# Optimization experiments

Measured on AMD Instinct MI355X. Metric: run time of the kernel, lower is better.

Reference implementation:

```python
import jax, jax.numpy as jnp
import numpy as np

WIN = 9
PAD = WIN // 2    # floor(9/2) = 4
WIN_SIZE = WIN * WIN
EPS = 1e-05


def _box_sum(x):
    # 9x9 ones-kernel conv, stride 1, pad 4 (SAME size), NCHW with C=1
    filt = jnp.ones((1, 1, WIN, WIN), dtype=x.dtype)
    return jax.lax.conv_general_dilated(
        x, filt, window_strides=(1, 1),
        padding=[(PAD, PAD), (PAD, PAD)],
        dimension_numbers=('NCHW', 'OIHW', 'NCHW'))


def setup_inputs() -> dict:
    key = jax.random.key(0)
    k1, k2 = jax.random.split(key)
    I = jax.random.normal(k1, (8, 1, 1024, 1024), dtype=jnp.float32)
    J = jax.random.normal(k2, (8, 1, 1024, 1024), dtype=jnp.float32)
    return {"I": I, "J": J}


def reference(I, J):
    I_sum = _box_sum(I)
    J_sum = _box_sum(J)
    I2_sum = _box_sum(I * I)
    J2_sum = _box_sum(J * J)
    IJ_sum = _box_sum(I * J)

    u_I = I_sum / WIN_SIZE
    u_J = J_sum / WIN_SIZE

    cross = IJ_sum - u_J * I_sum - u_I * J_sum + u_I * u_J * WIN_SIZE
    I_var = I2_sum - 2 * u_I * I_sum + u_I * u_I * WIN_SIZE
    J_var = J2_sum - 2 * u_J * J_sum + u_J * u_J * WIN_SIZE

    cc = cross * cross / (I_var * J_var + EPS)
    return jnp.mean(cc)
```

## Files before the change

kernel.cpp:

```cpp
#include <hip/hip_runtime.h>

#define H 1024
#define W 1024
#define NIMG 8
#define TX 64
#define CY 8
#define RS_ROWS (CY + 8)
#define NBX (W / TX)
#define NBY (H / CY)
#define NBLOCKS (NBX * NBY * NIMG)
#define EPS 1e-5f

__global__ __launch_bounds__(128, 4)
void ncc_main(const float* __restrict__ I, const float* __restrict__ J,
              float* __restrict__ partial) {
  __shared__ float4 rs4[RS_ROWS][TX];
  __shared__ float  rs1[RS_ROWS][TX];

  const int tid = threadIdx.x;
  const int gx = blockIdx.x, gy = blockIdx.y, n = blockIdx.z;
  const size_t img_off = (size_t)n * H * W;

  {
    const int r  = tid >> 3;
    const int xg = tid & 7;
    const int y  = gy * CY + r - 4;
    float a[16], b[16];
    if (y >= 0 && y < H) {
      const int xbase = gx * TX + xg * 8 - 4;
      const float* Ip = I + img_off + (size_t)y * W;
      const float* Jp = J + img_off + (size_t)y * W;
      if (xbase >= 0 && xbase + 16 <= W) {
        const float4* pa = reinterpret_cast<const float4*>(Ip + xbase);
        const float4* pb = reinterpret_cast<const float4*>(Jp + xbase);
        #pragma unroll
        for (int q = 0; q < 4; ++q) {
          float4 va = pa[q], vb = pb[q];
          a[4*q+0] = va.x; a[4*q+1] = va.y; a[4*q+2] = va.z; a[4*q+3] = va.w;
          b[4*q+0] = vb.x; b[4*q+1] = vb.y; b[4*q+2] = vb.z; b[4*q+3] = vb.w;
        }
      } else {
        #pragma unroll
        for (int k = 0; k < 16; ++k) {
          int xx = xbase + k;
          bool in = (xx >= 0) && (xx < W);
          a[k] = in ? Ip[xx] : 0.0f;
          b[k] = in ? Jp[xx] : 0.0f;
        }
      }
    } else {
      #pragma unroll
      for (int k = 0; k < 16; ++k) { a[k] = 0.0f; b[k] = 0.0f; }
    }
    float sI = 0.f, sJ = 0.f, sII = 0.f, sJJ = 0.f, sIJ = 0.f;
    #pragma unroll
    for (int k = 0; k < 9; ++k) {
      sI  += a[k];        sJ  += b[k];
      sII += a[k] * a[k]; sJJ += b[k] * b[k];
      sIJ += a[k] * b[k];
    }
    const int xg8 = xg * 8;
    #pragma unroll
    for (int i = 0; i < 8; ++i) {
      if (i > 0) {
        float an = a[i+8], al = a[i-1], bn = b[i+8], bl = b[i-1];
        sI  += an - al;           sJ  += bn - bl;
        sII += an*an - al*al;     sJJ += bn*bn - bl*bl;
        sIJ += an*bn - al*bl;
      }
      const int px = xg8 + (i ^ xg);
      rs4[r][px] = make_float4(sI, sJ, sII, sJJ);
      rs1[r][px] = sIJ;
    }
  }
  __syncthreads();

  const int x  = tid & 63;
  const int h  = tid >> 6;
  const int xs = (x & ~7) | ((x ^ (x >> 3)) & 7);
  const int base = h * 4;
  float4 rows4[9]; float rows1[9];
  float wI = 0.f, wJ = 0.f, wII = 0.f, wJJ = 0.f, wIJ = 0.f;
  #pragma unroll
  for (int k = 0; k < 9; ++k) {
    rows4[k] = rs4[base + k][xs];
    rows1[k] = rs1[base + k][xs];
    wI += rows4[k].x; wJ += rows4[k].y; wII += rows4[k].z; wJJ += rows4[k].w;
    wIJ += rows1[k];
  }
  const float inv81 = 1.0f / 81.0f;
  float acc = 0.f;
  #pragma unroll
  for (int i = 0; i < 4; ++i) {
    if (i > 0) {
      float4 e4 = rs4[base + 8 + i][xs];
      float  e1 = rs1[base + 8 + i][xs];
      wI  += e4.x - rows4[i-1].x;  wJ  += e4.y - rows4[i-1].y;
      wII += e4.z - rows4[i-1].z;  wJJ += e4.w - rows4[i-1].w;
      wIJ += e1   - rows1[i-1];
    }
    float cross = fmaf(-(wI * wJ), inv81, wIJ);
    float Iv    = fmaf(-(wI * wI), inv81, wII);
    float Jv    = fmaf(-(wJ * wJ), inv81, wJJ);
    acc = fmaf(cross * cross,
               __builtin_amdgcn_rcpf(fmaf(Iv, Jv, EPS)), acc);
  }

  #pragma unroll
  for (int off = 32; off > 0; off >>= 1)
    acc += __shfl_down(acc, off, 64);
  __syncthreads();
  if ((tid & 63) == 0) rs1[0][tid >> 6] = acc;
  __syncthreads();
  if (tid == 0) {
    const int blin = blockIdx.x + NBX * (blockIdx.y + NBY * (int)blockIdx.z);
    partial[blin] = rs1[0][0] + rs1[0][1];
  }
}

__global__ __launch_bounds__(256)
void ncc_reduce(const float* __restrict__ partial, float* __restrict__ out) {
  __shared__ float red[4];
  const int tid = threadIdx.x;
  float s = 0.f;
  #pragma unroll 8
  for (int i = tid; i < NBLOCKS; i += 256) s += partial[i];
  #pragma unroll
  for (int off = 32; off > 0; off >>= 1)
    s += __shfl_down(s, off, 64);
  if ((tid & 63) == 0) red[tid >> 6] = s;
  __syncthreads();
  if (tid == 0)
    out[0] = (red[0] + red[1] + red[2] + red[3]) *
             (1.0f / (float)((size_t)NIMG * H * W));
}

extern "C" void kernel_launch(void* const* d_in, const int* in_sizes, int n_in,
                              void* d_out, int out_size, void* d_ws, size_t ws_size,
                              hipStream_t stream) {
  const float* I = (const float*)d_in[0];
  const float* J = (const float*)d_in[1];
  float* out     = (float*)d_out;
  float* partial = (float*)d_ws;

  dim3 grid(NBX, NBY, NIMG);
  hipLaunchKernelGGL(ncc_main, grid, dim3(128), 0, stream, I, J, partial);
  hipLaunchKernelGGL(ncc_reduce, dim3(1), dim3(256), 0, stream, partial, out);
}
```

Measured before the change: 112.6 us.

## Process eight row tiles per block with register double-buffered global loads

Each block now loops over eight consecutive 8-row tiles instead of handling one, which cuts the grid by eight. The global loads for the next tile are issued into a second register buffer before the current tile's horizontal and vertical sums run, so memory latency overlaps compute. The 16-row halo is still re-read for every tile, so halo traffic does not shrink. The change adds a second barrier per tile and doubles the load registers, which may reduce occupancy, and the smaller grid may leave some CUs less busy.

Result: slower. 132.1 us (+17.3%).

```diff
diff --git a/kernel.cpp b/kernel.cpp
--- a/kernel.cpp
+++ b/kernel.cpp
@@ -5,111 +5,137 @@
 #define NIMG 8
 #define TX 64
 #define CY 8
-#define RS_ROWS (CY + 8)
+#define TPB 8
 #define NBX (W / TX)
-#define NBY (H / CY)
+#define NBY (H / (CY * TPB))
 #define NBLOCKS (NBX * NBY * NIMG)
 #define EPS 1e-5f
+
+__device__ __forceinline__ void load16(const float* __restrict__ Ip,
+                                       const float* __restrict__ Jp,
+                                       int y, int xbase, bool xfast,
+                                       float* __restrict__ a,
+                                       float* __restrict__ b) {
+  if (y >= 0 && y < H) {
+    const float* Irow = Ip + (size_t)y * W;
+    const float* Jrow = Jp + (size_t)y * W;
+    if (xfast) {
+      const float4* pa = reinterpret_cast<const float4*>(Irow + xbase);
+      const float4* pb = reinterpret_cast<const float4*>(Jrow + xbase);
+      #pragma unroll
+      for (int q = 0; q < 4; ++q) {
+        float4 va = pa[q], vb = pb[q];
+        a[4*q+0]=va.x; a[4*q+1]=va.y; a[4*q+2]=va.z; a[4*q+3]=va.w;
+        b[4*q+0]=vb.x; b[4*q+1]=vb.y; b[4*q+2]=vb.z; b[4*q+3]=vb.w;
+      }
+    } else {
+      #pragma unroll
+      for (int k = 0; k < 16; ++k) {
+        int xx = xbase + k;
+        bool in = (xx >= 0) && (xx < W);
+        a[k] = in ? Irow[xx] : 0.0f;
+        b[k] = in ? Jrow[xx] : 0.0f;
+      }
+    }
+  } else {
+    #pragma unroll
+    for (int k = 0; k < 16; ++k) { a[k] = 0.0f; b[k] = 0.0f; }
+  }
+}
 
 __global__ __launch_bounds__(128, 4)
 void ncc_main(const float* __restrict__ I, const float* __restrict__ J,
               float* __restrict__ partial) {
-  __shared__ float4 rs4[RS_ROWS][TX];
-  __shared__ float  rs1[RS_ROWS][TX];
+  __shared__ float4 rs4[16][TX];
+  __shared__ float  rs1[16][TX];
 
   const int tid = threadIdx.x;
   const int gx = blockIdx.x, gy = blockIdx.y, n = blockIdx.z;
   const size_t img_off = (size_t)n * H * W;
+  const float* Ip = I + img_off;
+  const float* Jp = J + img_off;
 
-  {
-    const int r  = tid >> 3;
-    const int xg = tid & 7;
-    const int y  = gy * CY + r - 4;
-    float a[16], b[16];
-    if (y >= 0 && y < H) {
-      const int xbase = gx * TX + xg * 8 - 4;
-      const float* Ip = I + img_off + (size_t)y * W;
-      const float* Jp = J + img_off + (size_t)y * W;
-      if (xbase >= 0 && xbase + 16 <= W) {
-        const float4* pa = reinterpret_cast<const float4*>(Ip + xbase);
-        const float4* pb = reinterpret_cast<const float4*>(Jp + xbase);
-        #pragma unroll
-        for (int q = 0; q < 4; ++q) {
-          float4 va = pa[q], vb = pb[q];
-          a[4*q+0] = va.x; a[4*q+1] = va.y; a[4*q+2] = va.z; a[4*q+3] = va.w;
-          b[4*q+0] = vb.x; b[4*q+1] = vb.y; b[4*q+2] = vb.z; b[4*q+3] = vb.w;
-        }
-      } else {
-        #pragma unroll
-        for (int k = 0; k < 16; ++k) {
-          int xx = xbase + k;
-          bool in = (xx >= 0) && (xx < W);
-          a[k] = in ? Ip[xx] : 0.0f;
-          b[k] = in ? Jp[xx] : 0.0f;
-        }
-      }
-    } else {
-      #pragma unroll
-      for (int k = 0; k < 16; ++k) { a[k] = 0.0f; b[k] = 0.0f; }
-    }
-    float sI = 0.f, sJ = 0.f, sII = 0.f, sJJ = 0.f, sIJ = 0.f;
-    #pragma unroll
-    for (int k = 0; k < 9; ++k) {
-      sI  += a[k];        sJ  += b[k];
-      sII += a[k] * a[k]; sJJ += b[k] * b[k];
-      sIJ += a[k] * b[k];
-    }
-    const int xg8 = xg * 8;
-    #pragma unroll
-    for (int i = 0; i < 8; ++i) {
-      if (i > 0) {
-        float an = a[i+8], al = a[i-1], bn = b[i+8], bl = b[i-1];
-        sI  += an - al;           sJ  += bn - bl;
-        sII += an*an - al*al;     sJJ += bn*bn - bl*bl;
-        sIJ += an*bn - al*bl;
-      }
-      const int px = xg8 + (i ^ xg);
-      rs4[r][px] = make_float4(sI, sJ, sII, sJJ);
-      rs1[r][px] = sIJ;
-    }
-  }
-  __syncthreads();
+  const int r  = tid >> 3;
+  const int xg = tid & 7;
+  const int xg8 = xg * 8;
+  const int xbase = gx * TX + xg8 - 4;
+  const bool xfast = (xbase >= 0) && (xbase + 16 <= W);
+  const int x  = tid & 63;
+  const int hh = tid >> 6;
+  const int xs = (x & ~7) | ((x ^ (x >> 3)) & 7);
+  const int pbase = hh * 4;
 
-  const int x  = tid & 63;
-  const int h  = tid >> 6;
-  const int xs = (x & ~7) | ((x ^ (x >> 3)) & 7);
-  const int base = h * 4;
-  float4 rows4[9]; float rows1[9];
-  float wI = 0.f, wJ = 0.f, wII = 0.f, wJJ = 0.f, wIJ = 0.f;
-  #pragma unroll
-  for (int k = 0; k < 9; ++k) {
-    rows4[k] = rs4[base + k][xs];
-    rows1[k] = rs1[base + k][xs];
-    wI += rows4[k].x; wJ += rows4[k].y; wII += rows4[k].z; wJJ += rows4[k].w;
-    wIJ += rows1[k];
-  }
+  const int y0 = gy * (CY * TPB);
+  float abuf[2][16], bbuf[2][16];
+  load16(Ip, Jp, y0 + r - 4, xbase, xfast, abuf[0], bbuf[0]);
+
   const float inv81 = 1.0f / 81.0f;
   float acc = 0.f;
+
   #pragma unroll
-  for (int i = 0; i < 4; ++i) {
-    if (i > 0) {
-      float4 e4 = rs4[base + 8 + i][xs];
-      float  e1 = rs1[base + 8 + i][xs];
-      wI  += e4.x - rows4[i-1].x;  wJ  += e4.y - rows4[i-1].y;
-      wII += e4.z - rows4[i-1].z;  wJJ += e4.w - rows4[i-1].w;
-      wIJ += e1   - rows1[i-1];
+  for (int t = 0; t < TPB; ++t) {
+    const int cb = t & 1, nb = cb ^ 1;
+    if (t < TPB - 1)
+      load16(Ip, Jp, y0 + (t+1)*CY + r - 4, xbase, xfast, abuf[nb], bbuf[nb]);
+
+    {
+      const float* a = abuf[cb];
+      const float* b = bbuf[cb];
+      float sI=0.f, sJ=0.f, sII=0.f, sJJ=0.f, sIJ=0.f;
+      #pragma unroll
+      for (int k = 0; k < 9; ++k) {
+        sI  += a[k];        sJ  += b[k];
+        sII += a[k]*a[k];   sJJ += b[k]*b[k];
+        sIJ += a[k]*b[k];
+      }
+      #pragma unroll
+      for (int i = 0; i < 8; ++i) {
+        if (i > 0) {
+          float an=a[i+8], al=a[i-1], bn=b[i+8], bl=b[i-1];
+          sI  += an - al;         sJ  += bn - bl;
+          sII += an*an - al*al;   sJJ += bn*bn - bl*bl;
+          sIJ += an*bn - al*bl;
+        }
+        const int px = xg8 + (i ^ xg);
+        rs4[r][px] = make_float4(sI, sJ, sII, sJJ);
+        rs1[r][px] = sIJ;
+      }
     }
-    float cross = fmaf(-(wI * wJ), inv81, wIJ);
-    float Iv    = fmaf(-(wI * wI), inv81, wII);
-    float Jv    = fmaf(-(wJ * wJ), inv81, wJJ);
-    acc = fmaf(cross * cross,
-               __builtin_amdgcn_rcpf(fmaf(Iv, Jv, EPS)), acc);
+    __syncthreads();
+
+    {
+      float4 rows4[9]; float rows1[9];
+      float wI=0.f, wJ=0.f, wII=0.f, wJJ=0.f, wIJ=0.f;
+      #pragma unroll
+      for (int k = 0; k < 9; ++k) {
+        rows4[k] = rs4[pbase + k][xs];
+        rows1[k] = rs1[pbase + k][xs];
+        wI += rows4[k].x; wJ += rows4[k].y;
+        wII += rows4[k].z; wJJ += rows4[k].w;
+        wIJ += rows1[k];
+      }
+      #pragma unroll
+      for (int i = 0; i < 4; ++i) {
+        if (i > 0) {
+          float4 e4 = rs4[pbase + 8 + i][xs];
+          float  e1 = rs1[pbase + 8 + i][xs];
+          wI  += e4.x - rows4[i-1].x;  wJ  += e4.y - rows4[i-1].y;
+          wII += e4.z - rows4[i-1].z;  wJJ += e4.w - rows4[i-1].w;
+          wIJ += e1   - rows1[i-1];
+        }
+        float cross = fmaf(-(wI * wJ), inv81, wIJ);
+        float Iv    = fmaf(-(wI * wI), inv81, wII);
+        float Jv    = fmaf(-(wJ * wJ), inv81, wJJ);
+        acc = fmaf(cross * cross,
+                   __builtin_amdgcn_rcpf(fmaf(Iv, Jv, EPS)), acc);
+      }
+    }
+    __syncthreads();
   }
 
   #pragma unroll
   for (int off = 32; off > 0; off >>= 1)
     acc += __shfl_down(acc, off, 64);
-  __syncthreads();
   if ((tid & 63) == 0) rs1[0][tid >> 6] = acc;
   __syncthreads();
   if (tid == 0) {
```
